# Kernel optimization log

Hardware: AMD Instinct MI355X
Metric: run time of the kernel (lower is better)

The kernel has to match this reference:

```python
import jax, jax.numpy as jnp
import numpy as np

N_NODES = 50000
N_EDGES = 800000
IN_CH, HID_CH, OUT_CH = 256, 128, 64


def setup_inputs() -> dict:
    key = jax.random.key(0)
    k_x, k_e, k_w1, k_w2 = jax.random.split(key, 4)
    x = jax.random.normal(k_x, (N_NODES, IN_CH), dtype=jnp.float32)
    edge_index = jax.random.randint(k_e, (2, N_EDGES), 0, N_NODES, dtype=jnp.int32)
    # Glorot-style init like PyG GCNConv (weight [in, out], bias zeros)
    s1 = float(np.sqrt(6.0 / (IN_CH + HID_CH)))
    s2 = float(np.sqrt(6.0 / (HID_CH + OUT_CH)))
    W1 = jax.random.uniform(k_w1, (IN_CH, HID_CH), jnp.float32, -s1, s1)
    b1 = jnp.zeros((HID_CH,), jnp.float32)
    W2 = jax.random.uniform(k_w2, (HID_CH, OUT_CH), jnp.float32, -s2, s2)
    b2 = jnp.zeros((OUT_CH,), jnp.float32)
    return {"x": x, "edge_index": edge_index, "W1": W1, "b1": b1, "W2": W2, "b2": b2}


def _gcn_conv(x, src, dst, deg_inv_sqrt, W, b, n_nodes):
    """GCNConv with self-loops: D^{-1/2}(A+I)D^{-1/2} X W + b."""
    h = x @ W  # [N, out]
    norm = deg_inv_sqrt[src] * deg_inv_sqrt[dst]          # [E]
    msgs = h[src] * norm[:, None]                          # [E, out] gather
    agg = jax.ops.segment_sum(msgs, dst, num_segments=n_nodes)  # scatter-add
    self_loop = h * (deg_inv_sqrt * deg_inv_sqrt)[:, None]      # self-loop term
    return agg + self_loop + b


def reference(x, edge_index, W1, b1, W2, b2):
    n = x.shape[0]
    src, dst = edge_index[0], edge_index[1]
    # degree includes self-loop (+1), edge weight 1, counted at destination
    deg = jnp.zeros((n,), x.dtype).at[dst].add(1.0) + 1.0
    dis = jax.lax.rsqrt(deg)
    h = jax.nn.relu(_gcn_conv(x, src, dst, dis, W1, b1, n))
    out = jax.nn.relu(_gcn_conv(h, src, dst, dis, W2, b2, n))
    return out
```

## Files before the change

### kernel.cpp

```cpp
#include <hip/hip_runtime.h>

#define N_NODES 50000
#define N_EDGES 800000
#define IN_CH 256
#define HID_CH 128
#define OUT_CH 64
#define CAP 64
#define NBINS 196
#define PCHUNK 3200
#define PBLOCKS 250
#define SWZ_ELEMS (IN_CH * HID_CH + HID_CH * OUT_CH)
#define SWZ_BLOCKS (SWZ_ELEMS / 256)

typedef _Float16 f16;
typedef _Float16 f16x8 __attribute__((ext_vector_type(8)));
typedef float f32x4 __attribute__((ext_vector_type(4)));
typedef unsigned short u16;
typedef unsigned int u32;

template <int K, int N>
__device__ __forceinline__ void swz(const float* __restrict__ W, f16* __restrict__ Bsw,
                                    int idx) {
    constexpr int NTILES = N / 16;
    int j = idx & 7;
    int lane = (idx >> 3) & 63;
    int rest = idx >> 9;
    int nt = rest % NTILES;
    int ks = rest / NTILES;
    int k = ks * 32 + (lane >> 4) * 8 + j;
    int n = nt * 16 + (lane & 15);
    Bsw[idx] = (f16)W[(size_t)k * N + n];
}

__device__ __forceinline__ void scan_local(const int* __restrict__ binCnt,
                                           int* sc, int* vv) {
    const int t = threadIdx.x;
    int v = (t < NBINS) ? binCnt[t] : 0;
    sc[t] = v; vv[t] = v;
    __syncthreads();
    for (int ofs = 1; ofs < 256; ofs <<= 1) {
        int add = (t >= ofs) ? sc[t - ofs] : 0;
        __syncthreads();
        sc[t] += add;
        __syncthreads();
    }
}

__global__ __launch_bounds__(256) void k_pre(const int* __restrict__ dst,
                                             int* __restrict__ binCnt,
                                             const float* __restrict__ W1,
                                             const float* __restrict__ W2,
                                             f16* __restrict__ B1,
                                             f16* __restrict__ B2) {
    if ((int)blockIdx.x < PBLOCKS) {
        __shared__ int lcnt[NBINS];
        for (int i = threadIdx.x; i < NBINS; i += 256) lcnt[i] = 0;
        __syncthreads();
        int base = blockIdx.x * PCHUNK;
        for (int i = base + (int)threadIdx.x; i < base + PCHUNK; i += 256)
            atomicAdd(&lcnt[dst[i] >> 8], 1);
        __syncthreads();
        for (int i = threadIdx.x; i < NBINS; i += 256)
            if (lcnt[i]) atomicAdd(&binCnt[i], lcnt[i]);
        return;
    }
    int idx = ((int)blockIdx.x - PBLOCKS) * 256 + threadIdx.x;
    if (idx < IN_CH * HID_CH) {
        swz<IN_CH, HID_CH>(W1, B1, idx);
    } else {
        idx -= IN_CH * HID_CH;
        if (idx < HID_CH * OUT_CH) swz<HID_CH, OUT_CH>(W2, B2, idx);
    }
}

__global__ __launch_bounds__(256) void k_place(const int* __restrict__ src,
                                               const int* __restrict__ dst,
                                               const int* __restrict__ binCnt,
                                               int* __restrict__ binCursor,
                                               u32* __restrict__ ebuf, int E) {
    __shared__ u32 codes[PCHUNK];
    __shared__ int sc[256], vv[256];
    __shared__ int lcnt[NBINS], lbase[NBINS], lcur[NBINS];
    scan_local(binCnt, sc, vv);
    for (int i = threadIdx.x; i < NBINS; i += 256) lcnt[i] = 0;
    __syncthreads();
    int base = blockIdx.x * PCHUNK;
    int m = min(PCHUNK, E - base);
    for (int j = threadIdx.x; j < m; j += 256) {
        u32 d = (u32)dst[base + j];
        codes[j] = (d << 16) | (u32)src[base + j];
        atomicAdd(&lcnt[d >> 8], 1);
    }
    __syncthreads();
    for (int i = threadIdx.x; i < NBINS; i += 256) {
        lbase[i] = (sc[i] - vv[i]) + atomicAdd(&binCursor[i], lcnt[i]);
        lcur[i] = 0;
    }
    __syncthreads();
    for (int j = threadIdx.x; j < m; j += 256) {
        u32 c = codes[j];
        int b = c >> 24;
        int p = atomicAdd(&lcur[b], 1);
        ebuf[lbase[b] + p] = c;
    }
}

__global__ __launch_bounds__(256) void k_build(const u32* __restrict__ ebuf,
                                               const int* __restrict__ binCnt,
                                               int* __restrict__ cnt,
                                               float* __restrict__ dis,
                                               u16* __restrict__ bucket, int N) {
    __shared__ int sc[256], vv[256];
    __shared__ int lcnt[256];
    __shared__ u16 lbuck[256 * CAP];
    scan_local(binCnt, sc, vv);
    int t = threadIdx.x;
    lcnt[t] = 0;
    __syncthreads();
    int b = blockIdx.x;
    int s = sc[b] - vv[b];
    int e = sc[b];
    for (int i = s + t; i < e; i += 256) {
        u32 c = ebuf[i];
        int local = (c >> 16) & 255;
        int p = atomicAdd(&lcnt[local], 1);
        if (p < CAP) lbuck[local * CAP + p] = (u16)(c & 0xFFFFu);
    }
    __syncthreads();
    int nodeBase = b << 8;
    if (nodeBase + t < N) {
        cnt[nodeBase + t] = lcnt[t];
        dis[nodeBase + t] = rsqrtf((float)lcnt[t] + 1.0f);
    }
    const uint4* lsrc = (const uint4*)lbuck;
    uint4* gdst = (uint4*)(bucket + (size_t)nodeBase * CAP);
    for (int idx = t; idx < 256 * CAP / 8; idx += 256) {
        int row = idx >> 3;
        if (nodeBase + row < N) gdst[idx] = lsrc[idx];
    }
}

template <int K, int N, bool A_FP32, bool RELU>
__global__ __launch_bounds__(256) void k_gemm(const void* __restrict__ Av,
                                              const f16* __restrict__ Bsw,
                                              const float* __restrict__ dis,
                                              f16* __restrict__ C, int M) {
    constexpr int KSTEPS = K / 32, NTILES = N / 16;
    const int tid = threadIdx.x;
    const int wave = tid >> 6, lane = tid & 63;
    const int quad = lane >> 4, l16 = lane & 15;
    int row = blockIdx.x * 64 + wave * 16 + l16;
    const int rowc = row < M ? row : M - 1;

    f32x4 acc[NTILES];
#pragma unroll
    for (int t = 0; t < NTILES; ++t) acc[t] = (f32x4){0.f, 0.f, 0.f, 0.f};

#pragma unroll
    for (int ks = 0; ks < KSTEPS; ++ks) {
        f16x8 afrag;
        if (A_FP32) {
            const float* A = (const float*)Av;
            const float4* p = (const float4*)(A + (size_t)rowc * K + ks * 32 + quad * 8);
            float4 v0 = p[0], v1 = p[1];
            afrag[0] = (f16)v0.x; afrag[1] = (f16)v0.y;
            afrag[2] = (f16)v0.z; afrag[3] = (f16)v0.w;
            afrag[4] = (f16)v1.x; afrag[5] = (f16)v1.y;
            afrag[6] = (f16)v1.z; afrag[7] = (f16)v1.w;
        } else {
            const f16* A = (const f16*)Av;
            afrag = *(const f16x8*)(A + (size_t)rowc * K + ks * 32 + quad * 8);
            if (RELU) {
#pragma unroll
                for (int j = 0; j < 8; ++j)
                    afrag[j] = afrag[j] > (f16)0 ? afrag[j] : (f16)0;
            }
        }
#pragma unroll
        for (int t = 0; t < NTILES; ++t) {
            f16x8 bfrag = *(const f16x8*)(Bsw + (((size_t)ks * NTILES + t) * 64 + lane) * 8);
            acc[t] = __builtin_amdgcn_mfma_f32_16x16x32_f16(afrag, bfrag, acc[t], 0, 0, 0);
        }
    }

    int rbase = blockIdx.x * 64 + wave * 16 + quad * 4;
#pragma unroll
    for (int r = 0; r < 4; ++r) {
        int gr = rbase + r;
        if (gr < M) {
            float d = dis[gr];
#pragma unroll
            for (int t = 0; t < NTILES; ++t)
                C[(size_t)gr * N + t * 16 + l16] = (f16)(acc[t][r] * d);
        }
    }
}

__global__ __launch_bounds__(256) void k_pull1(const f16* __restrict__ g1,
                                               const float* __restrict__ dis,
                                               const float* __restrict__ b1,
                                               const int* __restrict__ cnt,
                                               const u16* __restrict__ bucket,
                                               f16* __restrict__ agg1) {
    int gtid = blockIdx.x * 256 + threadIdx.x;
    int u = gtid >> 4;
    int sub = gtid & 15;
    if (u >= N_NODES) return;
    const f16* gp = g1 + sub * 8;

    f16x8 sv = *(const f16x8*)(gp + (size_t)u * HID_CH);
    float a[8];
#pragma unroll
    for (int j = 0; j < 8; ++j) a[j] = (float)sv[j];

    int n = cnt[u];
    if (n > CAP) n = CAP;
    const u16* row = bucket + u * CAP;

    int k = 0;
    for (; k + 8 <= n; k += 8) {
        uint4 iv = *(const uint4*)(row + k);
        int s0 = iv.x & 0xFFFF, s1 = iv.x >> 16;
        int s2 = iv.y & 0xFFFF, s3 = iv.y >> 16;
        int s4 = iv.z & 0xFFFF, s5 = iv.z >> 16;
        int s6 = iv.w & 0xFFFF, s7 = iv.w >> 16;
        f16x8 v0 = *(const f16x8*)(gp + (size_t)s0 * HID_CH);
        f16x8 v1 = *(const f16x8*)(gp + (size_t)s1 * HID_CH);
        f16x8 v2 = *(const f16x8*)(gp + (size_t)s2 * HID_CH);
        f16x8 v3 = *(const f16x8*)(gp + (size_t)s3 * HID_CH);
        f16x8 v4 = *(const f16x8*)(gp + (size_t)s4 * HID_CH);
        f16x8 v5 = *(const f16x8*)(gp + (size_t)s5 * HID_CH);
        f16x8 v6 = *(const f16x8*)(gp + (size_t)s6 * HID_CH);
        f16x8 v7 = *(const f16x8*)(gp + (size_t)s7 * HID_CH);
#pragma unroll
        for (int j = 0; j < 8; ++j)
            a[j] += (((float)v0[j] + (float)v1[j]) + ((float)v2[j] + (float)v3[j])) +
                    (((float)v4[j] + (float)v5[j]) + ((float)v6[j] + (float)v7[j]));
    }
    if (k + 4 <= n) {
        ushort4 s4v = *(const ushort4*)(row + k);
        f16x8 v0 = *(const f16x8*)(gp + (size_t)s4v.x * HID_CH);
        f16x8 v1 = *(const f16x8*)(gp + (size_t)s4v.y * HID_CH);
        f16x8 v2 = *(const f16x8*)(gp + (size_t)s4v.z * HID_CH);
        f16x8 v3 = *(const f16x8*)(gp + (size_t)s4v.w * HID_CH);
#pragma unroll
        for (int j = 0; j < 8; ++j)
            a[j] += ((float)v0[j] + (float)v1[j]) + ((float)v2[j] + (float)v3[j]);
        k += 4;
    }
    for (; k < n; ++k) {
        f16x8 v = *(const f16x8*)(gp + (size_t)row[k] * HID_CH);
#pragma unroll
        for (int j = 0; j < 8; ++j) a[j] += (float)v[j];
    }

    float du = dis[u];
    f16x8 o;
#pragma unroll
    for (int j = 0; j < 8; ++j) o[j] = (f16)fmaf(du, a[j], b1[sub * 8 + j]);
    *(f16x8*)(agg1 + (size_t)u * HID_CH + sub * 8) = o;
}

__global__ __launch_bounds__(256) void k_pull2(const f16* __restrict__ g2,
                                               const float* __restrict__ dis,
                                               const float* __restrict__ b2,
                                               const int* __restrict__ cnt,
                                               const u16* __restrict__ bucket,
                                               float* __restrict__ out) {
    int gtid = blockIdx.x * 256 + threadIdx.x;
    int u = gtid >> 3;
    int sub = gtid & 7;
    if (u >= N_NODES) return;
    const f16* gp = g2 + sub * 8;

    f16x8 sv = *(const f16x8*)(gp + (size_t)u * OUT_CH);
    float a[8];
#pragma unroll
    for (int j = 0; j < 8; ++j) a[j] = (float)sv[j];

    int n = cnt[u];
    if (n > CAP) n = CAP;
    const u16* row = bucket + u * CAP;

    int k = 0;
    for (; k + 8 <= n; k += 8) {
        uint4 iv = *(const uint4*)(row + k);
        int s0 = iv.x & 0xFFFF, s1 = iv.x >> 16;
        int s2 = iv.y & 0xFFFF, s3 = iv.y >> 16;
        int s4 = iv.z & 0xFFFF, s5 = iv.z >> 16;
        int s6 = iv.w & 0xFFFF, s7 = iv.w >> 16;
        f16x8 v0 = *(const f16x8*)(gp + (size_t)s0 * OUT_CH);
        f16x8 v1 = *(const f16x8*)(gp + (size_t)s1 * OUT_CH);
        f16x8 v2 = *(const f16x8*)(gp + (size_t)s2 * OUT_CH);
        f16x8 v3 = *(const f16x8*)(gp + (size_t)s3 * OUT_CH);
        f16x8 v4 = *(const f16x8*)(gp + (size_t)s4 * OUT_CH);
        f16x8 v5 = *(const f16x8*)(gp + (size_t)s5 * OUT_CH);
        f16x8 v6 = *(const f16x8*)(gp + (size_t)s6 * OUT_CH);
        f16x8 v7 = *(const f16x8*)(gp + (size_t)s7 * OUT_CH);
#pragma unroll
        for (int j = 0; j < 8; ++j)
            a[j] += (((float)v0[j] + (float)v1[j]) + ((float)v2[j] + (float)v3[j])) +
                    (((float)v4[j] + (float)v5[j]) + ((float)v6[j] + (float)v7[j]));
    }
    if (k + 4 <= n) {
        ushort4 s4v = *(const ushort4*)(row + k);
        f16x8 v0 = *(const f16x8*)(gp + (size_t)s4v.x * OUT_CH);
        f16x8 v1 = *(const f16x8*)(gp + (size_t)s4v.y * OUT_CH);
        f16x8 v2 = *(const f16x8*)(gp + (size_t)s4v.z * OUT_CH);
        f16x8 v3 = *(const f16x8*)(gp + (size_t)s4v.w * OUT_CH);
#pragma unroll
        for (int j = 0; j < 8; ++j)
            a[j] += ((float)v0[j] + (float)v1[j]) + ((float)v2[j] + (float)v3[j]);
        k += 4;
    }
    for (; k < n; ++k) {
        f16x8 v = *(const f16x8*)(gp + (size_t)row[k] * OUT_CH);
#pragma unroll
        for (int j = 0; j < 8; ++j) a[j] += (float)v[j];
    }

    float du = dis[u];
    float4* op = (float4*)(out + (size_t)u * OUT_CH + sub * 8);
    float4 o0, o1;
    o0.x = fmaxf(fmaf(du, a[0], b2[sub * 8 + 0]), 0.f);
    o0.y = fmaxf(fmaf(du, a[1], b2[sub * 8 + 1]), 0.f);
    o0.z = fmaxf(fmaf(du, a[2], b2[sub * 8 + 2]), 0.f);
    o0.w = fmaxf(fmaf(du, a[3], b2[sub * 8 + 3]), 0.f);
    o1.x = fmaxf(fmaf(du, a[4], b2[sub * 8 + 4]), 0.f);
    o1.y = fmaxf(fmaf(du, a[5], b2[sub * 8 + 5]), 0.f);
    o1.z = fmaxf(fmaf(du, a[6], b2[sub * 8 + 6]), 0.f);
    o1.w = fmaxf(fmaf(du, a[7], b2[sub * 8 + 7]), 0.f);
    op[0] = o0;
    op[1] = o1;
}


extern "C" void kernel_launch(void* const* d_in, const int* in_sizes, int n_in,
                              void* d_out, int out_size, void* d_ws, size_t ws_size,
                              hipStream_t stream) {
    const float* x  = (const float*)d_in[0];
    const int* ei   = (const int*)d_in[1];
    const float* W1 = (const float*)d_in[2];
    const float* b1 = (const float*)d_in[3];
    const float* W2 = (const float*)d_in[4];
    const float* b2 = (const float*)d_in[5];
    float* out = (float*)d_out;

    const int* src = ei;
    const int* dst = ei + N_EDGES;

    char* ws = (char*)d_ws;
    size_t off = 0;
    auto alloc = [&](size_t bytes) -> void* {
        off = (off + 255) & ~(size_t)255;
        void* p = ws + off;
        off += bytes;
        return p;
    };
    int*   zbuf      = (int*)alloc((size_t)(NBINS * 2) * 4);
    int*   binCnt    = zbuf;
    int*   binCursor = zbuf + NBINS;
    u32*   ebuf      = (u32*)alloc((size_t)N_EDGES * 4);
    int*   cnt       = (int*)alloc((size_t)N_NODES * 4);
    float* dis       = (float*)alloc((size_t)N_NODES * 4);
    u16*   bucket    = (u16*)alloc((size_t)N_NODES * CAP * 2);
    f16*   W1sw      = (f16*)alloc((size_t)IN_CH * HID_CH * 2);
    f16*   W2sw      = (f16*)alloc((size_t)HID_CH * OUT_CH * 2);
    f16*   g1        = (f16*)alloc((size_t)N_NODES * HID_CH * 2);
    f16*   agg1      = (f16*)alloc((size_t)N_NODES * HID_CH * 2);
    f16*   g2        = (f16*)alloc((size_t)N_NODES * OUT_CH * 2);

    hipMemsetAsync(zbuf, 0, (size_t)(NBINS * 2) * 4, stream);

    k_pre<<<PBLOCKS + SWZ_BLOCKS, 256, 0, stream>>>(dst, binCnt, W1, W2, W1sw, W2sw);
    k_place<<<PBLOCKS, 256, 0, stream>>>(src, dst, binCnt, binCursor, ebuf, N_EDGES);
    k_build<<<NBINS, 256, 0, stream>>>(ebuf, binCnt, cnt, dis, bucket, N_NODES);

    k_gemm<IN_CH, HID_CH, true, false><<<(N_NODES + 63) / 64, 256, 0, stream>>>(
        x, W1sw, dis, g1, N_NODES);

    k_pull1<<<(N_NODES * 16 + 255) / 256, 256, 0, stream>>>(g1, dis, b1, cnt, bucket, agg1);

    k_gemm<HID_CH, OUT_CH, false, true><<<(N_NODES + 63) / 64, 256, 0, stream>>>(
        agg1, W2sw, dis, g2, N_NODES);

    k_pull2<<<(N_NODES * 8 + 255) / 256, 256, 0, stream>>>(g2, dis, b2, cnt, bucket, out);
}
```

Baseline: 202.9 us.

## Fuse layer-1 aggregation with layer-2 GEMM via LDS tile; skip empty bucket writes

The layer-1 neighbor pull and the second GEMM now run in one kernel. Each block aggregates 64 nodes into an LDS tile, applies bias and ReLU there, then runs MFMA against W2. This removes the agg1 global round trip and one kernel launch. The bucket build also skips copying 16-byte chunks beyond each node's edge count, which cuts write traffic. The cost is fewer threads per node in the gather phase (4 iterations per thread) and lower parallelism, since the grid goes from 3125 blocks to 782.

```diff
diff --git a/kernel.cpp b/kernel.cpp
--- a/kernel.cpp
+++ b/kernel.cpp
@@ -136,7 +136,8 @@
     uint4* gdst = (uint4*)(bucket + (size_t)nodeBase * CAP);
     for (int idx = t; idx < 256 * CAP / 8; idx += 256) {
         int row = idx >> 3;
-        if (nodeBase + row < N) gdst[idx] = lsrc[idx];
+        int chunk = idx & 7;
+        if (nodeBase + row < N && (chunk << 3) < lcnt[row]) gdst[idx] = lsrc[idx];
     }
 }
 
@@ -196,69 +197,120 @@
     }
 }
 
-__global__ __launch_bounds__(256) void k_pull1(const f16* __restrict__ g1,
-                                               const float* __restrict__ dis,
-                                               const float* __restrict__ b1,
-                                               const int* __restrict__ cnt,
-                                               const u16* __restrict__ bucket,
-                                               f16* __restrict__ agg1) {
-    int gtid = blockIdx.x * 256 + threadIdx.x;
-    int u = gtid >> 4;
-    int sub = gtid & 15;
-    if (u >= N_NODES) return;
-    const f16* gp = g1 + sub * 8;
-
-    f16x8 sv = *(const f16x8*)(gp + (size_t)u * HID_CH);
-    float a[8];
-#pragma unroll
-    for (int j = 0; j < 8; ++j) a[j] = (float)sv[j];
-
-    int n = cnt[u];
-    if (n > CAP) n = CAP;
-    const u16* row = bucket + u * CAP;
-
-    int k = 0;
-    for (; k + 8 <= n; k += 8) {
-        uint4 iv = *(const uint4*)(row + k);
-        int s0 = iv.x & 0xFFFF, s1 = iv.x >> 16;
-        int s2 = iv.y & 0xFFFF, s3 = iv.y >> 16;
-        int s4 = iv.z & 0xFFFF, s5 = iv.z >> 16;
-        int s6 = iv.w & 0xFFFF, s7 = iv.w >> 16;
-        f16x8 v0 = *(const f16x8*)(gp + (size_t)s0 * HID_CH);
-        f16x8 v1 = *(const f16x8*)(gp + (size_t)s1 * HID_CH);
-        f16x8 v2 = *(const f16x8*)(gp + (size_t)s2 * HID_CH);
-        f16x8 v3 = *(const f16x8*)(gp + (size_t)s3 * HID_CH);
-        f16x8 v4 = *(const f16x8*)(gp + (size_t)s4 * HID_CH);
-        f16x8 v5 = *(const f16x8*)(gp + (size_t)s5 * HID_CH);
-        f16x8 v6 = *(const f16x8*)(gp + (size_t)s6 * HID_CH);
-        f16x8 v7 = *(const f16x8*)(gp + (size_t)s7 * HID_CH);
-#pragma unroll
-        for (int j = 0; j < 8; ++j)
-            a[j] += (((float)v0[j] + (float)v1[j]) + ((float)v2[j] + (float)v3[j])) +
-                    (((float)v4[j] + (float)v5[j]) + ((float)v6[j] + (float)v7[j]));
-    }
-    if (k + 4 <= n) {
-        ushort4 s4v = *(const ushort4*)(row + k);
-        f16x8 v0 = *(const f16x8*)(gp + (size_t)s4v.x * HID_CH);
-        f16x8 v1 = *(const f16x8*)(gp + (size_t)s4v.y * HID_CH);
-        f16x8 v2 = *(const f16x8*)(gp + (size_t)s4v.z * HID_CH);
-        f16x8 v3 = *(const f16x8*)(gp + (size_t)s4v.w * HID_CH);
-#pragma unroll
-        for (int j = 0; j < 8; ++j)
-            a[j] += ((float)v0[j] + (float)v1[j]) + ((float)v2[j] + (float)v3[j]);
-        k += 4;
-    }
-    for (; k < n; ++k) {
-        f16x8 v = *(const f16x8*)(gp + (size_t)row[k] * HID_CH);
-#pragma unroll
-        for (int j = 0; j < 8; ++j) a[j] += (float)v[j];
-    }
-
-    float du = dis[u];
-    f16x8 o;
-#pragma unroll
-    for (int j = 0; j < 8; ++j) o[j] = (f16)fmaf(du, a[j], b1[sub * 8 + j]);
-    *(f16x8*)(agg1 + (size_t)u * HID_CH + sub * 8) = o;
+__global__ __launch_bounds__(256) void k_pullgemm(const f16* __restrict__ g1,
+                                                  const float* __restrict__ dis,
+                                                  const float* __restrict__ b1,
+                                                  const int* __restrict__ cnt,
+                                                  const u16* __restrict__ bucket,
+                                                  const f16* __restrict__ B2sw,
+                                                  f16* __restrict__ g2) {
+    constexpr int LDSW = HID_CH + 8;
+    __shared__ f16 aggl[64 * LDSW];
+    const int tid = threadIdx.x;
+    const int sub = tid & 15;
+    const int nl = tid >> 4;
+    const int blockBase = (int)blockIdx.x * 64;
+
+    const float4* b1p = (const float4*)(b1 + sub * 8);
+    float4 bb0 = b1p[0], bb1 = b1p[1];
+    float bv[8] = {bb0.x, bb0.y, bb0.z, bb0.w, bb1.x, bb1.y, bb1.z, bb1.w};
+
+    for (int it = 0; it < 4; ++it) {
+        int lrow = it * 16 + nl;
+        int u = blockBase + lrow;
+        f16x8 o;
+        if (u < N_NODES) {
+            const f16* gp = g1 + sub * 8;
+            f16x8 sv = *(const f16x8*)(gp + (size_t)u * HID_CH);
+            float a[8];
+#pragma unroll
+            for (int j = 0; j < 8; ++j) a[j] = (float)sv[j];
+
+            int n = cnt[u];
+            if (n > CAP) n = CAP;
+            const u16* row = bucket + u * CAP;
+
+            int k = 0;
+            for (; k + 8 <= n; k += 8) {
+                uint4 iv = *(const uint4*)(row + k);
+                int s0 = iv.x & 0xFFFF, s1 = iv.x >> 16;
+                int s2 = iv.y & 0xFFFF, s3 = iv.y >> 16;
+                int s4 = iv.z & 0xFFFF, s5 = iv.z >> 16;
+                int s6 = iv.w & 0xFFFF, s7 = iv.w >> 16;
+                f16x8 v0 = *(const f16x8*)(gp + (size_t)s0 * HID_CH);
+                f16x8 v1 = *(const f16x8*)(gp + (size_t)s1 * HID_CH);
+                f16x8 v2 = *(const f16x8*)(gp + (size_t)s2 * HID_CH);
+                f16x8 v3 = *(const f16x8*)(gp + (size_t)s3 * HID_CH);
+                f16x8 v4 = *(const f16x8*)(gp + (size_t)s4 * HID_CH);
+                f16x8 v5 = *(const f16x8*)(gp + (size_t)s5 * HID_CH);
+                f16x8 v6 = *(const f16x8*)(gp + (size_t)s6 * HID_CH);
+                f16x8 v7 = *(const f16x8*)(gp + (size_t)s7 * HID_CH);
+#pragma unroll
+                for (int j = 0; j < 8; ++j)
+                    a[j] += (((float)v0[j] + (float)v1[j]) + ((float)v2[j] + (float)v3[j])) +
+                            (((float)v4[j] + (float)v5[j]) + ((float)v6[j] + (float)v7[j]));
+            }
+            if (k + 4 <= n) {
+                ushort4 s4v = *(const ushort4*)(row + k);
+                f16x8 v0 = *(const f16x8*)(gp + (size_t)s4v.x * HID_CH);
+                f16x8 v1 = *(const f16x8*)(gp + (size_t)s4v.y * HID_CH);
+                f16x8 v2 = *(const f16x8*)(gp + (size_t)s4v.z * HID_CH);
+                f16x8 v3 = *(const f16x8*)(gp + (size_t)s4v.w * HID_CH);
+#pragma unroll
+                for (int j = 0; j < 8; ++j)
+                    a[j] += ((float)v0[j] + (float)v1[j]) + ((float)v2[j] + (float)v3[j]);
+                k += 4;
+            }
+            for (; k < n; ++k) {
+                f16x8 v = *(const f16x8*)(gp + (size_t)row[k] * HID_CH);
+#pragma unroll
+                for (int j = 0; j < 8; ++j) a[j] += (float)v[j];
+            }
+
+            float du = dis[u];
+#pragma unroll
+            for (int j = 0; j < 8; ++j) {
+                float t = fmaf(du, a[j], bv[j]);
+                o[j] = (f16)(t > 0.f ? t : 0.f);
+            }
+        } else {
+#pragma unroll
+            for (int j = 0; j < 8; ++j) o[j] = (f16)0;
+        }
+        *(f16x8*)(aggl + (size_t)lrow * LDSW + sub * 8) = o;
+    }
+    __syncthreads();
+
+    constexpr int KSTEPS = HID_CH / 32, NTILES = OUT_CH / 16;
+    const int wave = tid >> 6, lane = tid & 63;
+    const int quad = lane >> 4, l16 = lane & 15;
+    const int lrowA = wave * 16 + l16;
+
+    f32x4 acc[NTILES];
+#pragma unroll
+    for (int t = 0; t < NTILES; ++t) acc[t] = (f32x4){0.f, 0.f, 0.f, 0.f};
+
+#pragma unroll
+    for (int ks = 0; ks < KSTEPS; ++ks) {
+        f16x8 afrag = *(const f16x8*)(aggl + (size_t)lrowA * LDSW + ks * 32 + quad * 8);
+#pragma unroll
+        for (int t = 0; t < NTILES; ++t) {
+            f16x8 bfrag = *(const f16x8*)(B2sw + (((size_t)ks * NTILES + t) * 64 + lane) * 8);
+            acc[t] = __builtin_amdgcn_mfma_f32_16x16x32_f16(afrag, bfrag, acc[t], 0, 0, 0);
+        }
+    }
+
+    int rbase = blockBase + wave * 16 + quad * 4;
+#pragma unroll
+    for (int r = 0; r < 4; ++r) {
+        int gr = rbase + r;
+        if (gr < N_NODES) {
+            float d = dis[gr];
+#pragma unroll
+            for (int t = 0; t < NTILES; ++t)
+                g2[(size_t)gr * OUT_CH + t * 16 + l16] = (f16)(acc[t][r] * d);
+        }
+    }
 }
 
 __global__ __launch_bounds__(256) void k_pull2(const f16* __restrict__ g2,
@@ -367,7 +419,6 @@
     f16*   W1sw      = (f16*)alloc((size_t)IN_CH * HID_CH * 2);
     f16*   W2sw      = (f16*)alloc((size_t)HID_CH * OUT_CH * 2);
     f16*   g1        = (f16*)alloc((size_t)N_NODES * HID_CH * 2);
-    f16*   agg1      = (f16*)alloc((size_t)N_NODES * HID_CH * 2);
     f16*   g2        = (f16*)alloc((size_t)N_NODES * OUT_CH * 2);
 
     hipMemsetAsync(zbuf, 0, (size_t)(NBINS * 2) * 4, stream);
@@ -379,10 +430,8 @@
     k_gemm<IN_CH, HID_CH, true, false><<<(N_NODES + 63) / 64, 256, 0, stream>>>(
         x, W1sw, dis, g1, N_NODES);
 
-    k_pull1<<<(N_NODES * 16 + 255) / 256, 256, 0, stream>>>(g1, dis, b1, cnt, bucket, agg1);
-
-    k_gemm<HID_CH, OUT_CH, false, true><<<(N_NODES + 63) / 64, 256, 0, stream>>>(
-        agg1, W2sw, dis, g2, N_NODES);
+    k_pullgemm<<<(N_NODES + 63) / 64, 256, 0, stream>>>(g1, dis, b1, cnt, bucket,
+                                                        W2sw, g2);
 
     k_pull2<<<(N_NODES * 8 + 255) / 256, 256, 0, stream>>>(g2, dis, b2, cnt, bucket, out);
 }
```

Result: faster. 198.5 us (-2.2%).
